# Kernel optimization log

Hardware: AMD Instinct MI355X
Metric: run time of the kernel (lower is better)

## Reference

```python
import jax, jax.numpy as jnp
import numpy as np

DIM = 128
POS_HID = 64
ATTN_HID = DIM * 4
K_NEIGH = 16


def _mlp2(x, w1, b1, w2, b2):
    # Linear -> ReLU -> Linear (weights stored as (in, out))
    return jax.nn.relu(x @ w1 + b1) @ w2 + b2


def setup_inputs() -> dict:
    key = jax.random.key(0)
    ks = jax.random.split(key, 12)
    B, N = 2, 512
    s = 0.05
    return {
        "x": jax.random.normal(ks[0], (B, DIM, N), jnp.float32),
        "pos": jax.random.normal(ks[1], (B, N, 3), jnp.float32),
        "w_qkv": jax.random.normal(ks[2], (DIM, 3 * DIM), jnp.float32) * s,
        "pos_w1": jax.random.normal(ks[3], (3, POS_HID), jnp.float32) * s,
        "pos_b1": jnp.zeros((POS_HID,), jnp.float32),
        "pos_w2": jax.random.normal(ks[4], (POS_HID, DIM), jnp.float32) * s,
        "pos_b2": jnp.zeros((DIM,), jnp.float32),
        "attn_w1": jax.random.normal(ks[5], (DIM, ATTN_HID), jnp.float32) * s,
        "attn_b1": jnp.zeros((ATTN_HID,), jnp.float32),
        "attn_w2": jax.random.normal(ks[6], (ATTN_HID, DIM), jnp.float32) * s,
        "attn_b2": jnp.zeros((DIM,), jnp.float32),
    }


def reference(x, pos, w_qkv, pos_w1, pos_b1, pos_w2, pos_b2,
              attn_w1, attn_b1, attn_w2, attn_b2):
    # x: (B, dim, N) -> (B, N, dim)
    xt = jnp.swapaxes(x, 1, 2)
    B, N, d = xt.shape

    qkv = xt @ w_qkv                           # (B, N, 3d), no bias
    q, k, v = jnp.split(qkv, 3, axis=-1)

    rel_pos = pos[:, :, None, :] - pos[:, None, :, :]          # (B, N, N, 3)
    rel_pos_emb = _mlp2(rel_pos, pos_w1, pos_b1, pos_w2, pos_b2)  # (B, N, N, d)
    qk_rel = q[:, :, None, :] - k[:, None, :, :]               # (B, N, N, d)

    # KNN: smallest euclidean rel distances per query point
    rel_dist = jnp.sqrt(jnp.sum(rel_pos * rel_pos, axis=-1))   # (B, N, N)
    _, idx = jax.lax.top_k(-rel_dist, K_NEIGH)                 # (B, N, K)

    idxe = idx[..., None]                                      # (B, N, K, 1)
    v_g = v[jnp.arange(B)[:, None, None], idx]                 # (B, N, K, d)
    qk_g = jnp.take_along_axis(qk_rel, idxe, axis=2)           # (B, N, K, d)
    pe_g = jnp.take_along_axis(rel_pos_emb, idxe, axis=2)      # (B, N, K, d)

    v_g = v_g + pe_g
    sim = _mlp2(qk_g + pe_g, attn_w1, attn_b1, attn_w2, attn_b2)  # (B, N, K, d)
    attn = jax.nn.softmax(sim, axis=-2)                        # softmax over neighbors
    agg = jnp.einsum('bikd,bikd->bid', attn, v_g)              # (B, N, d)
    return jnp.swapaxes(agg, 1, 2)                             # (B, d, N)
```

## Files before the change

kernel.cpp:

```cpp
#include <hip/hip_runtime.h>
#include <math.h>

#define DIM 128
#define N_PTS 512
#define K_NEIGH 16
#define POS_HID 64
#define ATTN_HID 512

typedef __attribute__((ext_vector_type(8))) short short8;
typedef __attribute__((ext_vector_type(4))) float f32x4;
typedef unsigned short us;
typedef unsigned long long ull;

__device__ __forceinline__ us f2b(float f) {
    unsigned int u = __builtin_bit_cast(unsigned int, f);
    u += 0x7fffu + ((u >> 16) & 1u);
    return (us)(u >> 16);
}

__device__ __forceinline__ ull shflx64(ull v, int m) {
    int lo = __shfl_xor((int)(unsigned int)v, m);
    int hi = __shfl_xor((int)(unsigned int)(v >> 32), m);
    return ((ull)(unsigned int)hi << 32) | (unsigned int)lo;
}

__global__ void pack_kernel(const float* __restrict__ wqkv,
                            const float* __restrict__ aw1,
                            const float* __restrict__ aw2,
                            const float* __restrict__ pw2,
                            us* __restrict__ p0, us* __restrict__ p1,
                            us* __restrict__ p2, us* __restrict__ p3) {
    int t = blockIdx.x * 256 + threadIdx.x;
    if (t < 49152) {
        int j = t & 7, l = (t >> 3) & 63, rem = t >> 9;
        int nt = rem % 24, ks = rem / 24;
        int k = ks * 32 + (l >> 4) * 8 + j, n = nt * 16 + (l & 15);
        p0[t] = f2b(wqkv[k * 384 + n]);
    } else if (t < 114688) {
        int u = t - 49152;
        int j = u & 7, l = (u >> 3) & 63, nt = (u >> 9) & 31, ks = u >> 14;
        int k = ks * 32 + (l >> 4) * 8 + j, n = nt * 16 + (l & 15);
        p1[u] = f2b(aw1[k * ATTN_HID + n]);
    } else if (t < 180224) {
        int u = t - 114688;
        int j = u & 7, l = (u >> 3) & 63, nt = (u >> 9) & 7, ch = u >> 12;
        int k = ch * 32 + (l >> 4) * 8 + j, n = nt * 16 + (l & 15);
        p2[u] = f2b(aw2[k * DIM + n]);
    } else if (t < 188416) {
        int u = t - 180224;
        int j = u & 7, l = (u >> 3) & 63, nt = (u >> 9) & 7, ks = u >> 12;
        int k = ks * 32 + (l >> 4) * 8 + j, n = nt * 16 + (l & 15);
        p3[u] = f2b(pw2[k * DIM + n]);
    }
}

__global__ __launch_bounds__(256)
void qkv_mfma_kernel(const float* __restrict__ x,
                     const us* __restrict__ p0,
                     float* __restrict__ qkv) {
    __shared__ __align__(16) us xA[16][136];
    const int tid = threadIdx.x;
    const int w = tid >> 6, lane = tid & 63, quad = lane >> 4, lq = lane & 15;
    const int n0 = blockIdx.x * 16;
    const int b = n0 >> 9, nn = n0 & (N_PTS - 1);
#pragma unroll
    for (int rr = 0; rr < 8; ++rr) {
        int id = rr * 256 + tid;
        int d = id >> 4, i = id & 15;
        xA[i][d] = f2b(x[(size_t)(b * DIM + d) * N_PTS + nn + i]);
    }
    __syncthreads();
    short8 a[4];
#pragma unroll
    for (int ks = 0; ks < 4; ++ks)
        a[ks] = *(const short8*)&xA[lq][ks * 32 + quad * 8];
#pragma unroll
    for (int i = 0; i < 6; ++i) {
        int nt = w * 6 + i;
        f32x4 acc = {0.f, 0.f, 0.f, 0.f};
#pragma unroll
        for (int ks = 0; ks < 4; ++ks) {
            const short8 bf = *(const short8*)(p0 + (size_t)((ks * 24 + nt) * 64 + lane) * 8);
            acc = __builtin_amdgcn_mfma_f32_16x16x32_bf16(a[ks], bf, acc, 0, 0, 0);
        }
#pragma unroll
        for (int r = 0; r < 4; ++r)
            qkv[(size_t)(n0 + quad * 4 + r) * 384 + nt * 16 + lq] = acc[r];
    }
}

__global__ __launch_bounds__(256)
void attn_fused_kernel(const float* __restrict__ pos,
                       const float* __restrict__ qkv,
                       const float* __restrict__ pw1,
                       const float* __restrict__ pb1,
                       const float* __restrict__ pb2,
                       const us* __restrict__ p1,
                       const us* __restrict__ p2,
                       const us* __restrict__ p3,
                       const float* __restrict__ ab1,
                       float* __restrict__ out) {
    __shared__ __align__(16) us hinA[4][16][136];
    __shared__ __align__(16) us h1s[4][16][40];
    __shared__ int nbrs[4][16];

    const int tid = threadIdx.x;
    const int w = tid >> 6, lane = tid & 63, quad = lane >> 4, lq = lane & 15;
    const int g = blockIdx.x * 4 + w, b = g >> 9, n = g & (N_PTS - 1);

    {
        const float pix = pos[g * 3 + 0], piy = pos[g * 3 + 1], piz = pos[g * 3 + 2];
        float d2[8];
#pragma unroll
        for (int rr = 0; rr < 8; ++rr) {
            int j = rr * 64 + lane;
            float dx = pix - pos[(b * N_PTS + j) * 3 + 0];
            float dy = piy - pos[(b * N_PTS + j) * 3 + 1];
            float dz = piz - pos[(b * N_PTS + j) * 3 + 2];
            d2[rr] = dx * dx + dy * dy + dz * dz;
        }
        for (int r = 0; r < K_NEIGH; ++r) {
            ull key = ~0ULL;
#pragma unroll
            for (int rr = 0; rr < 8; ++rr) {
                unsigned int fb = __builtin_bit_cast(unsigned int, d2[rr]);
                ull k2 = ((ull)fb << 32) | (unsigned int)(rr * 64 + lane);
                key = k2 < key ? k2 : key;
            }
#pragma unroll
            for (int off = 32; off > 0; off >>= 1) {
                ull o = shflx64(key, off);
                key = o < key ? o : key;
            }
            unsigned int jw = (unsigned int)key;
            if (lane == 0) nbrs[w][r] = (int)jw;
            if (lane == (int)(jw & 63)) d2[jw >> 6] = __builtin_inff();
        }
    }

    short8 pha[2];
    {
        const int jn = nbrs[w][lq];
        float rx = pos[g * 3 + 0] - pos[(b * N_PTS + jn) * 3 + 0];
        float ry = pos[g * 3 + 1] - pos[(b * N_PTS + jn) * 3 + 1];
        float rz = pos[g * 3 + 2] - pos[(b * N_PTS + jn) * 3 + 2];
#pragma unroll
        for (int ks = 0; ks < 2; ++ks) {
            short8 f;
#pragma unroll
            for (int jj = 0; jj < 8; ++jj) {
                int c = ks * 32 + quad * 8 + jj;
                float h = rx * pw1[c] + ry * pw1[64 + c] + rz * pw1[128 + c] + pb1[c];
                f[jj] = (short)f2b(fmaxf(h, 0.f));
            }
            pha[ks] = f;
        }
    }

    f32x4 pe[8];
#pragma unroll
    for (int nt = 0; nt < 8; ++nt) {
        const short8 b0 = *(const short8*)(p3 + (size_t)((0 * 8 + nt) * 64 + lane) * 8);
        const short8 b1 = *(const short8*)(p3 + (size_t)((1 * 8 + nt) * 64 + lane) * 8);
        f32x4 acc = {0.f, 0.f, 0.f, 0.f};
        acc = __builtin_amdgcn_mfma_f32_16x16x32_bf16(pha[0], b0, acc, 0, 0, 0);
        acc = __builtin_amdgcn_mfma_f32_16x16x32_bf16(pha[1], b1, acc, 0, 0, 0);
        float bias = pb2[nt * 16 + lq];
#pragma unroll
        for (int r = 0; r < 4; ++r) pe[nt][r] = acc[r] + bias;
    }

    f32x4 vg[8];
    {
        int jr[4];
#pragma unroll
        for (int r = 0; r < 4; ++r) jr[r] = nbrs[w][quad * 4 + r];
#pragma unroll
        for (int nt = 0; nt < 8; ++nt) {
            int d = nt * 16 + lq;
            float qv = qkv[(size_t)g * 384 + d];
#pragma unroll
            for (int r = 0; r < 4; ++r) {
                const float* kv = qkv + (size_t)(b * N_PTS + jr[r]) * 384;
                float pp = pe[nt][r];
                hinA[w][quad * 4 + r][d] = f2b(qv - kv[128 + d] + pp);
                vg[nt][r] = kv[256 + d] + pp;
            }
        }
    }

    short8 a1f[4];
#pragma unroll
    for (int ks = 0; ks < 4; ++ks)
        a1f[ks] = *(const short8*)&hinA[w][lq][ks * 32 + quad * 8];

    f32x4 c2[8];
#pragma unroll
    for (int nt = 0; nt < 8; ++nt) c2[nt] = (f32x4){0.f, 0.f, 0.f, 0.f};

    for (int ch = 0; ch < 16; ++ch) {
        short8 bf[2][4];
#pragma unroll
        for (int t = 0; t < 2; ++t)
#pragma unroll
            for (int ks = 0; ks < 4; ++ks)
                bf[t][ks] = *(const short8*)(p1 + (size_t)(((ks << 5) + ch * 2 + t) * 64 + lane) * 8);
#pragma unroll
        for (int t = 0; t < 2; ++t) {
            int nt = ch * 2 + t;
            f32x4 acc = {0.f, 0.f, 0.f, 0.f};
#pragma unroll
            for (int ks = 0; ks < 4; ++ks)
                acc = __builtin_amdgcn_mfma_f32_16x16x32_bf16(a1f[ks], bf[t][ks], acc, 0, 0, 0);
            float bias = ab1[nt * 16 + lq];
#pragma unroll
            for (int r = 0; r < 4; ++r)
                h1s[w][quad * 4 + r][t * 16 + lq] = f2b(fmaxf(acc[r] + bias, 0.f));
        }
        const short8 a2 = *(const short8*)&h1s[w][lq][quad * 8];
#pragma unroll
        for (int nt2 = 0; nt2 < 8; ++nt2) {
            const short8 bf2 = *(const short8*)(p2 + (size_t)(((ch << 3) + nt2) * 64 + lane) * 8);
            c2[nt2] = __builtin_amdgcn_mfma_f32_16x16x32_bf16(a2, bf2, c2[nt2], 0, 0, 0);
        }
    }

#pragma unroll
    for (int nt2 = 0; nt2 < 8; ++nt2) {
        f32x4 s4 = c2[nt2];
        float m = fmaxf(fmaxf(s4[0], s4[1]), fmaxf(s4[2], s4[3]));
        m = fmaxf(m, __shfl_xor(m, 16));
        m = fmaxf(m, __shfl_xor(m, 32));
        float e0 = __expf(s4[0] - m), e1 = __expf(s4[1] - m);
        float e2 = __expf(s4[2] - m), e3 = __expf(s4[3] - m);
        float s = e0 + e1 + e2 + e3;
        f32x4 v4 = vg[nt2];
        float a = e0 * v4[0] + e1 * v4[1] + e2 * v4[2] + e3 * v4[3];
        s += __shfl_xor(s, 16); s += __shfl_xor(s, 32);
        a += __shfl_xor(a, 16); a += __shfl_xor(a, 32);
        if (quad == 0)
            out[(size_t)(b * DIM + nt2 * 16 + lq) * N_PTS + n] = a / s;
    }
}

extern "C" void kernel_launch(void* const* d_in, const int* in_sizes, int n_in,
                              void* d_out, int out_size, void* d_ws, size_t ws_size,
                              hipStream_t stream) {
    const float* x    = (const float*)d_in[0];
    const float* pos  = (const float*)d_in[1];
    const float* wqkv = (const float*)d_in[2];
    const float* pw1  = (const float*)d_in[3];
    const float* pb1  = (const float*)d_in[4];
    const float* pw2  = (const float*)d_in[5];
    const float* pb2  = (const float*)d_in[6];
    const float* aw1  = (const float*)d_in[7];
    const float* ab1  = (const float*)d_in[8];
    const float* aw2  = (const float*)d_in[9];
    float* out = (float*)d_out;

    int B = in_sizes[0] / (DIM * N_PTS);
    int npts = B * N_PTS;

    char* ws = (char*)d_ws;
    float* qkv = (float*)ws;
    us* p0 = (us*)(ws + (size_t)npts * 384 * 4);
    us* p1 = p0 + 49152;
    us* p2 = p1 + 65536;
    us* p3 = p2 + 65536;

    pack_kernel<<<736, 256, 0, stream>>>(wqkv, aw1, aw2, pw2, p0, p1, p2, p3);
    qkv_mfma_kernel<<<npts / 16, 256, 0, stream>>>(x, p0, qkv);
    attn_fused_kernel<<<npts / 4, 256, 0, stream>>>(pos, qkv,
                                                    pw1, pb1, pb2,
                                                    p1, p2, p3, ab1, out);
}
```

Baseline: 115.2 us.

## Prefetch MLP weight fragments with double buffering and hoist loop-invariant loads

The attention kernel's 16-chunk MLP loop is fully unrolled and double-buffers the p1/p2 weight fragments in registers, so the next chunk's global loads overlap the current chunk's MFMAs. Position-MLP weights, biases, the p3 fragments and the query row are loaded before the KNN selection so their latency hides behind it. The QKV kernel moves to 512-thread blocks with 3 tiles per wave instead of 6. The extra live registers may lower occupancy or cause spills.

```diff
diff --git a/kernel.cpp b/kernel.cpp
--- a/kernel.cpp
+++ b/kernel.cpp
@@ -54,7 +54,7 @@
     }
 }
 
-__global__ __launch_bounds__(256)
+__global__ __launch_bounds__(512)
 void qkv_mfma_kernel(const float* __restrict__ x,
                      const us* __restrict__ p0,
                      float* __restrict__ qkv) {
@@ -64,8 +64,8 @@
     const int n0 = blockIdx.x * 16;
     const int b = n0 >> 9, nn = n0 & (N_PTS - 1);
 #pragma unroll
-    for (int rr = 0; rr < 8; ++rr) {
-        int id = rr * 256 + tid;
+    for (int rr = 0; rr < 4; ++rr) {
+        int id = rr * 512 + tid;
         int d = id >> 4, i = id & 15;
         xA[i][d] = f2b(x[(size_t)(b * DIM + d) * N_PTS + nn + i]);
     }
@@ -75,8 +75,8 @@
     for (int ks = 0; ks < 4; ++ks)
         a[ks] = *(const short8*)&xA[lq][ks * 32 + quad * 8];
 #pragma unroll
-    for (int i = 0; i < 6; ++i) {
-        int nt = w * 6 + i;
+    for (int i = 0; i < 3; ++i) {
+        int nt = w * 3 + i;
         f32x4 acc = {0.f, 0.f, 0.f, 0.f};
 #pragma unroll
         for (int ks = 0; ks < 4; ++ks) {
@@ -108,6 +108,32 @@
     const int w = tid >> 6, lane = tid & 63, quad = lane >> 4, lq = lane & 15;
     const int g = blockIdx.x * 4 + w, b = g >> 9, n = g & (N_PTS - 1);
 
+    short8 b3f[2][8];
+#pragma unroll
+    for (int ks = 0; ks < 2; ++ks)
+#pragma unroll
+        for (int nt = 0; nt < 8; ++nt)
+            b3f[ks][nt] = *(const short8*)(p3 + (size_t)((ks * 8 + nt) * 64 + lane) * 8);
+
+    float w1x[2][8], w1y[2][8], w1z[2][8], w1b[2][8];
+#pragma unroll
+    for (int ks = 0; ks < 2; ++ks)
+#pragma unroll
+        for (int jj = 0; jj < 8; ++jj) {
+            int c = ks * 32 + quad * 8 + jj;
+            w1x[ks][jj] = pw1[c];
+            w1y[ks][jj] = pw1[64 + c];
+            w1z[ks][jj] = pw1[128 + c];
+            w1b[ks][jj] = pb1[c];
+        }
+
+    float qvr[8], pb2r[8];
+#pragma unroll
+    for (int nt = 0; nt < 8; ++nt) {
+        qvr[nt]  = qkv[(size_t)g * 384 + nt * 16 + lq];
+        pb2r[nt] = pb2[nt * 16 + lq];
+    }
+
     {
         const float pix = pos[g * 3 + 0], piy = pos[g * 3 + 1], piz = pos[g * 3 + 2];
         float d2[8];
@@ -149,8 +175,7 @@
             short8 f;
 #pragma unroll
             for (int jj = 0; jj < 8; ++jj) {
-                int c = ks * 32 + quad * 8 + jj;
-                float h = rx * pw1[c] + ry * pw1[64 + c] + rz * pw1[128 + c] + pb1[c];
+                float h = rx * w1x[ks][jj] + ry * w1y[ks][jj] + rz * w1z[ks][jj] + w1b[ks][jj];
                 f[jj] = (short)f2b(fmaxf(h, 0.f));
             }
             pha[ks] = f;
@@ -160,14 +185,11 @@
     f32x4 pe[8];
 #pragma unroll
     for (int nt = 0; nt < 8; ++nt) {
-        const short8 b0 = *(const short8*)(p3 + (size_t)((0 * 8 + nt) * 64 + lane) * 8);
-        const short8 b1 = *(const short8*)(p3 + (size_t)((1 * 8 + nt) * 64 + lane) * 8);
         f32x4 acc = {0.f, 0.f, 0.f, 0.f};
-        acc = __builtin_amdgcn_mfma_f32_16x16x32_bf16(pha[0], b0, acc, 0, 0, 0);
-        acc = __builtin_amdgcn_mfma_f32_16x16x32_bf16(pha[1], b1, acc, 0, 0, 0);
-        float bias = pb2[nt * 16 + lq];
-#pragma unroll
-        for (int r = 0; r < 4; ++r) pe[nt][r] = acc[r] + bias;
+        acc = __builtin_amdgcn_mfma_f32_16x16x32_bf16(pha[0], b3f[0][nt], acc, 0, 0, 0);
+        acc = __builtin_amdgcn_mfma_f32_16x16x32_bf16(pha[1], b3f[1][nt], acc, 0, 0, 0);
+#pragma unroll
+        for (int r = 0; r < 4; ++r) pe[nt][r] = acc[r] + pb2r[nt];
     }
 
     f32x4 vg[8];
@@ -178,12 +200,11 @@
 #pragma unroll
         for (int nt = 0; nt < 8; ++nt) {
             int d = nt * 16 + lq;
-            float qv = qkv[(size_t)g * 384 + d];
 #pragma unroll
             for (int r = 0; r < 4; ++r) {
                 const float* kv = qkv + (size_t)(b * N_PTS + jr[r]) * 384;
                 float pp = pe[nt][r];
-                hinA[w][quad * 4 + r][d] = f2b(qv - kv[128 + d] + pp);
+                hinA[w][quad * 4 + r][d] = f2b(qvr[nt] - kv[128 + d] + pp);
                 vg[nt][r] = kv[256 + d] + pp;
             }
         }
@@ -198,31 +219,48 @@
 #pragma unroll
     for (int nt = 0; nt < 8; ++nt) c2[nt] = (f32x4){0.f, 0.f, 0.f, 0.f};
 
+    short8 p1f[2][2][4];
+    short8 p2f[2][8];
+#pragma unroll
+    for (int t = 0; t < 2; ++t)
+#pragma unroll
+        for (int ks = 0; ks < 4; ++ks)
+            p1f[0][t][ks] = *(const short8*)(p1 + (size_t)(((ks << 5) + t) * 64 + lane) * 8);
+#pragma unroll
+    for (int nt2 = 0; nt2 < 8; ++nt2)
+        p2f[0][nt2] = *(const short8*)(p2 + (size_t)(nt2 * 64 + lane) * 8);
+
+#pragma unroll
     for (int ch = 0; ch < 16; ++ch) {
-        short8 bf[2][4];
-#pragma unroll
-        for (int t = 0; t < 2; ++t)
-#pragma unroll
-            for (int ks = 0; ks < 4; ++ks)
-                bf[t][ks] = *(const short8*)(p1 + (size_t)(((ks << 5) + ch * 2 + t) * 64 + lane) * 8);
+        const int cur = ch & 1, nxt = cur ^ 1;
+        if (ch < 15) {
+#pragma unroll
+            for (int t = 0; t < 2; ++t)
+#pragma unroll
+                for (int ks = 0; ks < 4; ++ks)
+                    p1f[nxt][t][ks] = *(const short8*)(p1 + (size_t)(((ks << 5) + (ch + 1) * 2 + t) * 64 + lane) * 8);
+        }
 #pragma unroll
         for (int t = 0; t < 2; ++t) {
             int nt = ch * 2 + t;
             f32x4 acc = {0.f, 0.f, 0.f, 0.f};
 #pragma unroll
             for (int ks = 0; ks < 4; ++ks)
-                acc = __builtin_amdgcn_mfma_f32_16x16x32_bf16(a1f[ks], bf[t][ks], acc, 0, 0, 0);
+                acc = __builtin_amdgcn_mfma_f32_16x16x32_bf16(a1f[ks], p1f[cur][t][ks], acc, 0, 0, 0);
             float bias = ab1[nt * 16 + lq];
 #pragma unroll
             for (int r = 0; r < 4; ++r)
                 h1s[w][quad * 4 + r][t * 16 + lq] = f2b(fmaxf(acc[r] + bias, 0.f));
         }
+        if (ch < 15) {
+#pragma unroll
+            for (int nt2 = 0; nt2 < 8; ++nt2)
+                p2f[nxt][nt2] = *(const short8*)(p2 + (size_t)((((ch + 1) << 3) + nt2) * 64 + lane) * 8);
+        }
         const short8 a2 = *(const short8*)&h1s[w][lq][quad * 8];
 #pragma unroll
-        for (int nt2 = 0; nt2 < 8; ++nt2) {
-            const short8 bf2 = *(const short8*)(p2 + (size_t)(((ch << 3) + nt2) * 64 + lane) * 8);
-            c2[nt2] = __builtin_amdgcn_mfma_f32_16x16x32_bf16(a2, bf2, c2[nt2], 0, 0, 0);
-        }
+        for (int nt2 = 0; nt2 < 8; ++nt2)
+            c2[nt2] = __builtin_amdgcn_mfma_f32_16x16x32_bf16(a2, p2f[cur][nt2], c2[nt2], 0, 0, 0);
     }
 
 #pragma unroll
@@ -269,7 +307,7 @@
     us* p3 = p2 + 65536;
 
     pack_kernel<<<736, 256, 0, stream>>>(wqkv, aw1, aw2, pw2, p0, p1, p2, p3);
-    qkv_mfma_kernel<<<npts / 16, 256, 0, stream>>>(x, p0, qkv);
+    qkv_mfma_kernel<<<npts / 16, 512, 0, stream>>>(x, p0, qkv);
     attn_fused_kernel<<<npts / 4, 256, 0, stream>>>(pos, qkv,
                                                     pw1, pb1, pb2,
                                                     p1, p2, p3, ab1, out);
```

Measured after the change: 100.8 us. 1.14x faster.
